# Kernel tuning notes

Hardware: AMD Instinct MI355X
Metric: run time of the kernel (lower is better)

Reference implementation:

```python
import jax, jax.numpy as jnp
import numpy as np

DILS = [2 ** i for i in range(9)] * 7  # 27 residual-only layers + 36 layers with skip
N0 = 27  # first 27 layers (dilations0) do not contribute to skip connections


def _dconv(x, w, b, d):
    # dilated 'same' conv1d: x [B,C,T], w [O,I,3]
    y = jax.lax.conv_general_dilated(x, w, (1,), [(d, d)], rhs_dilation=(d,),
                                     dimension_numbers=('NCH', 'OIH', 'NCH'))
    return y + b[None, :, None]


def _pw(x, w, b):
    # 1x1 conv: w [O,C], x [B,C,T]
    return jnp.einsum('oc,bct->bot', w, x) + b[None, :, None]


def setup_inputs() -> dict:
    key = jax.random.key(0)
    ks = jax.random.split(key, 13)
    B, T, rd, sd, qd, L = 8, 16384, 128, 128, 256, 63
    s = 0.05
    f = lambda k, sh: jax.random.normal(k, sh, jnp.float32) * s
    return {
        'x': jax.random.normal(ks[0], (B, 1, T), jnp.float32),
        'causal_w': f(ks[1], (rd, 1, 25)),
        'causal_b': f(ks[2], (rd,)),
        'dcnn_w': f(ks[3], (L, rd, rd, 3)),
        'dcnn_b': f(ks[4], (L, rd)),
        'dense_w': f(ks[5], (L, rd, rd)),
        'dense_b': f(ks[6], (L, rd)),
        'skip_w': f(ks[7], (L, sd, rd)),
        'skip_b': f(ks[8], (L, sd)),
        'post1_w': f(ks[9], (sd, sd)),
        'post1_b': f(ks[10], (sd,)),
        'post2_w': f(ks[11], (qd, sd)),
        'post2_b': f(ks[12], (qd,)),
    }


def reference(x, causal_w, causal_b, dcnn_w, dcnn_b, dense_w, dense_b,
              skip_w, skip_b, post1_w, post1_b, post2_w, post2_b):
    # causal conv: kernel 25, padding 12 ('same')
    x = jax.lax.conv_general_dilated(x, causal_w, (1,), [(12, 12)],
                                     dimension_numbers=('NCH', 'OIH', 'NCH'))
    x = x + causal_b[None, :, None]
    B, _, T = x.shape
    skip = jnp.zeros((B, skip_w.shape[1], T), x.dtype)
    for cnt, d in enumerate(DILS):
        xin = x
        h = jax.nn.relu(x)
        h = jax.nn.relu(_dconv(h, dcnn_w[cnt], dcnn_b[cnt], d))
        if cnt >= N0:
            skip = skip + _pw(h, skip_w[cnt], skip_b[cnt])
        x = _pw(h, dense_w[cnt], dense_b[cnt]) + xin
    h = jax.nn.relu(_pw(jax.nn.relu(skip), post1_w, post1_b))
    return _pw(h, post2_w, post2_b)
```

## Files before the change

### kernel.cpp

```cpp
#include <hip/hip_runtime.h>

#define RD     128
#define TT     128
#define TLEN   16384
#define NB     8
#define NLAYER 63
#define N0SKIP 27
#define QD     256
#define PADR   136

typedef short bf16x8 __attribute__((ext_vector_type(8)));
typedef float f32x4  __attribute__((ext_vector_type(4)));

__device__ __forceinline__ unsigned short f2bf(float f) {
  unsigned u = __float_as_uint(f);
  u += 0x7fffu + ((u >> 16) & 1u);
  return (unsigned short)(u >> 16);
}
__device__ __forceinline__ short f2bf_relu(float f) {
  f = f > 0.f ? f : 0.f;
  unsigned u = __float_as_uint(f);
  u += 0x7fffu + ((u >> 16) & 1u);
  return (short)(u >> 16);
}

__device__ __forceinline__ void mfma_gemm(const unsigned short* __restrict__ aw,
                                          const short* sx, int rowbase,
                                          int c0w, int t0w, int n, int q,
                                          f32x4 (&acc)[4][4]) {
#pragma unroll
  for (int ks = 0; ks < 4; ++ks) {
    const int i0 = ks * 32 + q * 8;
    bf16x8 a[4], bb[4];
#pragma unroll
    for (int ct = 0; ct < 4; ++ct)
      a[ct] = *(const bf16x8*)&aw[(size_t)(c0w + ct * 16 + n) * RD + i0];
#pragma unroll
    for (int tt = 0; tt < 4; ++tt)
      bb[tt] = *(const bf16x8*)&sx[(rowbase + t0w + tt * 16 + n) * PADR + i0];
#pragma unroll
    for (int ct = 0; ct < 4; ++ct)
#pragma unroll
      for (int tt = 0; tt < 4; ++tt)
        acc[ct][tt] = __builtin_amdgcn_mfma_f32_16x16x32_bf16(a[ct], bb[tt],
                                                              acc[ct][tt], 0, 0, 0);
  }
}

__device__ __forceinline__ void zero_acc(f32x4 (&acc)[4][4]) {
#pragma unroll
  for (int i = 0; i < 4; ++i)
#pragma unroll
    for (int j = 0; j < 4; ++j) acc[i][j] = (f32x4){0.f, 0.f, 0.f, 0.f};
}

__device__ __forceinline__ void stage_rows(short* sx, int rowbase,
                                           const float* __restrict__ xb,
                                           int tstart, int nrows, int tid) {
  for (int idx = tid; idx < nrows * 32; idx += 256) {
    const int r = idx >> 5, c4 = (idx & 31) << 2;
    const int tg = tstart + r;
    float4 v = make_float4(0.f, 0.f, 0.f, 0.f);
    if ((unsigned)tg < (unsigned)TLEN)
      v = *(const float4*)&xb[(size_t)tg * RD + c4];
    short4 o;
    o.x = f2bf_relu(v.x); o.y = f2bf_relu(v.y);
    o.z = f2bf_relu(v.z); o.w = f2bf_relu(v.w);
    *(short4*)&sx[(rowbase + r) * PADR + c4] = o;
  }
}

__device__ __forceinline__ void store_act_bf16(short* dst, const f32x4 (&acc)[4][4],
                                               const float* __restrict__ bias,
                                               int c0w, int t0w, int n, int q) {
#pragma unroll
  for (int ct = 0; ct < 4; ++ct) {
    const int c = c0w + ct * 16 + q * 4;
    const float4 bb = *(const float4*)&bias[c];
#pragma unroll
    for (int tt = 0; tt < 4; ++tt) {
      const int t = t0w + tt * 16 + n;
      const f32x4 A = acc[ct][tt];
      short4 o;
      o.x = f2bf_relu(A[0] + bb.x);
      o.y = f2bf_relu(A[1] + bb.y);
      o.z = f2bf_relu(A[2] + bb.z);
      o.w = f2bf_relu(A[3] + bb.w);
      *(short4*)&dst[t * PADR + c] = o;
    }
  }
}

__device__ __forceinline__ void epi_accum(float* __restrict__ dst,
                                          const float* __restrict__ src,
                                          const float* __restrict__ bias,
                                          const f32x4 (&acc)[4][4],
                                          int c0w, int t0w, int n, int q) {
#pragma unroll
  for (int ct = 0; ct < 4; ++ct) {
    const int c = c0w + ct * 16 + q * 4;
    const float4 bb = *(const float4*)&bias[c];
#pragma unroll
    for (int tt = 0; tt < 4; ++tt) {
      const int t = t0w + tt * 16 + n;
      float4 r = *(const float4*)&src[(size_t)t * RD + c];
      const f32x4 A = acc[ct][tt];
      r.x += A[0] + bb.x; r.y += A[1] + bb.y;
      r.z += A[2] + bb.z; r.w += A[3] + bb.w;
      *(float4*)&dst[(size_t)t * RD + c] = r;
    }
  }
}

__global__ __launch_bounds__(256, 2) void layer_kernel(
    const float* __restrict__ x_in, float* __restrict__ x_out,
    float* __restrict__ skip,
    const unsigned short* __restrict__ wconv,
    const float* __restrict__ bconv,
    const unsigned short* __restrict__ wdense, const float* __restrict__ bdense,
    const unsigned short* __restrict__ wskip,  const float* __restrict__ bskip,
    int dil, int do_skip) {
  __shared__ short sx[256 * PADR];

  const int tid = threadIdx.x;
  const int b   = blockIdx.x >> 7;
  const int t0  = (blockIdx.x & 127) << 7;
  const int lane = tid & 63;
  const int n = lane & 15, q = lane >> 4;
  const int w = tid >> 6;
  const int c0w = (w & 1) * 64, t0w = (w >> 1) * 64;
  const float* xb = x_in + (size_t)b * TLEN * RD;

  f32x4 acc[4][4];
  zero_acc(acc);

  if (dil <= 64) {
    stage_rows(sx, 0, xb, t0 - dil, 128 + 2 * dil, tid);
    __syncthreads();
    for (int k = 0; k < 3; ++k)
      mfma_gemm(wconv + (size_t)k * RD * RD, sx, k * dil, c0w, t0w, n, q, acc);
  } else {
    stage_rows(sx, 0, xb, t0 - dil, 128, tid);
    __syncthreads();
    stage_rows(sx, 128, xb, t0, 128, tid);
    mfma_gemm(wconv, sx, 0, c0w, t0w, n, q, acc);
    __syncthreads();
    stage_rows(sx, 0, xb, t0 + dil, 128, tid);
    mfma_gemm(wconv + (size_t)RD * RD, sx, 128, c0w, t0w, n, q, acc);
    __syncthreads();
    mfma_gemm(wconv + (size_t)2 * RD * RD, sx, 0, c0w, t0w, n, q, acc);
  }
  __syncthreads();

  store_act_bf16(sx, acc, bconv, c0w, t0w, n, q);
  __syncthreads();

  zero_acc(acc);
  mfma_gemm(wdense, sx, 0, c0w, t0w, n, q, acc);
  {
    float* xo = x_out + ((size_t)b * TLEN + t0) * RD;
    const float* xi = x_in + ((size_t)b * TLEN + t0) * RD;
    epi_accum(xo, xi, bdense, acc, c0w, t0w, n, q);
  }

  if (do_skip) {
    zero_acc(acc);
    mfma_gemm(wskip, sx, 0, c0w, t0w, n, q, acc);
    float* sp = skip + ((size_t)b * TLEN + t0) * RD;
    epi_accum(sp, sp, bskip, acc, c0w, t0w, n, q);
  }
}

__global__ __launch_bounds__(256) void causal_kernel(const float* __restrict__ x,
                                                     const float* __restrict__ w,
                                                     const float* __restrict__ bias,
                                                     float* __restrict__ y) {
  __shared__ float xw[152];
  __shared__ float wl[RD * 25];
  __shared__ float bl[RD];
  const int tid = threadIdx.x;
  const int b   = blockIdx.x >> 7;
  const int t0  = (blockIdx.x & 127) << 7;
  for (int i = tid; i < RD * 25; i += 256) wl[i] = w[i];
  if (tid < RD) bl[tid] = bias[tid];
  for (int i = tid; i < 152; i += 256) {
    const int tg = t0 - 12 + i;
    xw[i] = ((unsigned)tg < (unsigned)TLEN) ? x[(size_t)b * TLEN + tg] : 0.f;
  }
  __syncthreads();
  const int c = tid & 127, tp = tid >> 7;
  float* yb = y + ((size_t)b * TLEN + t0) * RD + c;
  const float bc = bl[c];
  for (int i = 0; i < 64; ++i) {
    const int tl = i * 2 + tp;
    float s = bc;
#pragma unroll
    for (int k = 0; k < 25; ++k) s = fmaf(wl[c * 25 + k], xw[tl + k], s);
    yb[(size_t)tl * RD] = s;
  }
}

__global__ __launch_bounds__(256, 1) void post_kernel(
    const float* __restrict__ skip,
    const unsigned short* __restrict__ p1, const float* __restrict__ p1b,
    const unsigned short* __restrict__ p2, const float* __restrict__ p2b,
    float* __restrict__ out) {
  __shared__ short sb[128 * PADR];
  __shared__ short h1[128 * PADR];
  __shared__ float ost[128 * 132];

  const int tid = threadIdx.x;
  const int b   = blockIdx.x >> 7;
  const int t0  = (blockIdx.x & 127) << 7;
  const int lane = tid & 63;
  const int n = lane & 15, q = lane >> 4;
  const int w = tid >> 6;
  const int c0w = (w & 1) * 64, t0w = (w >> 1) * 64;
  const float* skb = skip + ((size_t)b * TLEN + t0) * RD;

  for (int idx = tid; idx < 128 * 32; idx += 256) {
    const int r = idx >> 5, c4 = (idx & 31) << 2;
    float4 v = *(const float4*)&skb[(size_t)r * RD + c4];
    short4 o;
    o.x = f2bf_relu(v.x); o.y = f2bf_relu(v.y);
    o.z = f2bf_relu(v.z); o.w = f2bf_relu(v.w);
    *(short4*)&sb[r * PADR + c4] = o;
  }
  __syncthreads();

  f32x4 acc[4][4];
  zero_acc(acc);
  mfma_gemm(p1, sb, 0, c0w, t0w, n, q, acc);
  store_act_bf16(h1, acc, p1b, c0w, t0w, n, q);
  __syncthreads();

  for (int half = 0; half < 2; ++half) {
    zero_acc(acc);
    mfma_gemm(p2 + (size_t)half * RD * RD, h1, 0, c0w, t0w, n, q, acc);
#pragma unroll
    for (int ct = 0; ct < 4; ++ct) {
      const int c = c0w + ct * 16 + q * 4;
      const float4 bb = *(const float4*)&p2b[half * RD + c];
#pragma unroll
      for (int tt = 0; tt < 4; ++tt) {
        const int t = t0w + tt * 16 + n;
        const f32x4 A = acc[ct][tt];
        ost[(c + 0) * 132 + t] = A[0] + bb.x;
        ost[(c + 1) * 132 + t] = A[1] + bb.y;
        ost[(c + 2) * 132 + t] = A[2] + bb.z;
        ost[(c + 3) * 132 + t] = A[3] + bb.w;
      }
    }
    __syncthreads();
    float* ob = out + ((size_t)b * QD + half * RD) * TLEN + t0;
    for (int idx = tid; idx < 128 * 32; idx += 256) {
      const int r = idx >> 5, t4 = (idx & 31) << 2;
      const float4 v = *(const float4*)&ost[r * 132 + t4];
      *(float4*)&ob[(size_t)r * TLEN + t4] = v;
    }
    __syncthreads();
  }
}

__global__ __launch_bounds__(256) void cvt_kernel(const float* __restrict__ in,
                                                  unsigned short* __restrict__ out,
                                                  int total) {
  const int i = blockIdx.x * 256 + threadIdx.x;
  if (i < total) out[i] = f2bf(in[i]);
}
__global__ __launch_bounds__(256) void cvt_conv_kernel(const float* __restrict__ in,
                                                       unsigned short* __restrict__ out,
                                                       int total) {
  const int idx = blockIdx.x * 256 + threadIdx.x;
  if (idx >= total) return;
  const int ci = idx & 127, co = (idx >> 7) & 127, lk = idx >> 14;
  const int k = lk % 3, l = lk / 3;
  out[idx] = f2bf(in[(((size_t)l * RD + co) * RD + ci) * 3 + k]);
}

extern "C" void kernel_launch(void* const* d_in, const int* in_sizes, int n_in,
                              void* d_out, int out_size, void* d_ws, size_t ws_size,
                              hipStream_t stream) {
  const float* x        = (const float*)d_in[0];
  const float* causal_w = (const float*)d_in[1];
  const float* causal_b = (const float*)d_in[2];
  const float* dcnn_w   = (const float*)d_in[3];
  const float* dcnn_b   = (const float*)d_in[4];
  const float* dense_w  = (const float*)d_in[5];
  const float* dense_b  = (const float*)d_in[6];
  const float* skip_w   = (const float*)d_in[7];
  const float* skip_b   = (const float*)d_in[8];
  const float* post1_w  = (const float*)d_in[9];
  const float* post1_b  = (const float*)d_in[10];
  const float* post2_w  = (const float*)d_in[11];
  const float* post2_b  = (const float*)d_in[12];
  float* out = (float*)d_out;

  const size_t XN = (size_t)NB * TLEN * RD;
  float* ws  = (float*)d_ws;
  float* xA  = ws;
  float* xB  = xA + XN;
  float* skp = xB + XN;
  unsigned short* wc  = (unsigned short*)(skp + XN);
  unsigned short* wd  = wc  + (size_t)NLAYER * 3 * RD * RD;
  unsigned short* wsk = wd  + (size_t)NLAYER * RD * RD;
  unsigned short* p1  = wsk + (size_t)NLAYER * RD * RD;
  unsigned short* p2  = p1  + RD * RD;

  const int tconv = NLAYER * 3 * RD * RD;
  const int t2    = NLAYER * RD * RD;
  cvt_conv_kernel<<<(tconv + 255) / 256, 256, 0, stream>>>(dcnn_w, wc, tconv);
  cvt_kernel<<<(t2 + 255) / 256, 256, 0, stream>>>(dense_w, wd, t2);
  cvt_kernel<<<(t2 + 255) / 256, 256, 0, stream>>>(skip_w, wsk, t2);
  cvt_kernel<<<(RD * RD + 255) / 256, 256, 0, stream>>>(post1_w, p1, RD * RD);
  cvt_kernel<<<(QD * RD + 255) / 256, 256, 0, stream>>>(post2_w, p2, QD * RD);

  causal_kernel<<<NB * (TLEN / TT), 256, 0, stream>>>(x, causal_w, causal_b, xA);
  hipMemsetAsync(skp, 0, XN * sizeof(float), stream);

  const float* src = xA;
  float* dst = xB;
  for (int l = 0; l < NLAYER; ++l) {
    const int dil = 1 << (l % 9);
    layer_kernel<<<NB * (TLEN / TT), 256, 0, stream>>>(
        src, dst, skp,
        wc  + (size_t)l * 3 * RD * RD, dcnn_b  + (size_t)l * RD,
        wd  + (size_t)l * RD * RD,     dense_b + (size_t)l * RD,
        wsk + (size_t)l * RD * RD,     skip_b  + (size_t)l * RD,
        dil, (l >= N0SKIP) ? 1 : 0);
    const float* tmp = src; src = dst; dst = (float*)tmp;
  }

  post_kernel<<<NB * (TLEN / TT), 256, 0, stream>>>(skp, p1, post1_b, p2, post2_b, out);
}
```

Measured before the change: 5.228 ms.

## Shrink LDS staging to raise occupancy, unroll staging loads, swizzle block order

Cuts the shared staging buffer from 256 to 192 rows and raises the launch-bounds occupancy hint from 2 to 3 blocks per CU. To fit, dilation 64 gets its own reuse-based staging path, and larger dilations stage one 128-row tap at a time with extra barriers. The staging loop is unrolled 8 ways so more global loads are in flight, and block IDs are swizzled across batches. The tighter launch bound may force register spills, and the added syncs for large dilations serialize load and compute.

```diff
diff --git a/kernel.cpp b/kernel.cpp
--- a/kernel.cpp
+++ b/kernel.cpp
@@ -8,6 +8,7 @@
 #define N0SKIP 27
 #define QD     256
 #define PADR   136
+#define SROWS  192
 
 typedef short bf16x8 __attribute__((ext_vector_type(8)));
 typedef float f32x4  __attribute__((ext_vector_type(4)));
@@ -54,19 +55,44 @@
     for (int j = 0; j < 4; ++j) acc[i][j] = (f32x4){0.f, 0.f, 0.f, 0.f};
 }
 
+#define SUNROLL 8
 __device__ __forceinline__ void stage_rows(short* sx, int rowbase,
                                            const float* __restrict__ xb,
                                            int tstart, int nrows, int tid) {
-  for (int idx = tid; idx < nrows * 32; idx += 256) {
-    const int r = idx >> 5, c4 = (idx & 31) << 2;
-    const int tg = tstart + r;
+  const int total = nrows * 32;
+  int idx = tid;
+  for (; idx + 256 * (SUNROLL - 1) < total; idx += 256 * SUNROLL) {
+    float4 v[SUNROLL];
+#pragma unroll
+    for (int u = 0; u < SUNROLL; ++u) {
+      const int i2 = idx + u * 256;
+      const int tg = tstart + (i2 >> 5);
+      const int c4 = (i2 & 31) << 2;
+      v[u] = make_float4(0.f, 0.f, 0.f, 0.f);
+      if ((unsigned)tg < (unsigned)TLEN)
+        v[u] = *(const float4*)&xb[(size_t)tg * RD + c4];
+    }
+#pragma unroll
+    for (int u = 0; u < SUNROLL; ++u) {
+      const int i2 = idx + u * 256;
+      const int r = i2 >> 5;
+      const int c4 = (i2 & 31) << 2;
+      short4 o;
+      o.x = f2bf_relu(v[u].x); o.y = f2bf_relu(v[u].y);
+      o.z = f2bf_relu(v[u].z); o.w = f2bf_relu(v[u].w);
+      *(short4*)&sx[(rowbase + r) * PADR + c4] = o;
+    }
+  }
+  for (; idx < total; idx += 256) {
+    const int tg = tstart + (idx >> 5);
+    const int c4 = (idx & 31) << 2;
     float4 v = make_float4(0.f, 0.f, 0.f, 0.f);
     if ((unsigned)tg < (unsigned)TLEN)
       v = *(const float4*)&xb[(size_t)tg * RD + c4];
     short4 o;
     o.x = f2bf_relu(v.x); o.y = f2bf_relu(v.y);
     o.z = f2bf_relu(v.z); o.w = f2bf_relu(v.w);
-    *(short4*)&sx[(rowbase + r) * PADR + c4] = o;
+    *(short4*)&sx[(rowbase + (idx >> 5)) * PADR + c4] = o;
   }
 }
 
@@ -112,7 +138,7 @@
   }
 }
 
-__global__ __launch_bounds__(256, 2) void layer_kernel(
+__global__ __launch_bounds__(256, 3) void layer_kernel(
     const float* __restrict__ x_in, float* __restrict__ x_out,
     float* __restrict__ skip,
     const unsigned short* __restrict__ wconv,
@@ -120,11 +146,13 @@
     const unsigned short* __restrict__ wdense, const float* __restrict__ bdense,
     const unsigned short* __restrict__ wskip,  const float* __restrict__ bskip,
     int dil, int do_skip) {
-  __shared__ short sx[256 * PADR];
+  __shared__ short sx[SROWS * PADR];
 
   const int tid = threadIdx.x;
-  const int b   = blockIdx.x >> 7;
-  const int t0  = (blockIdx.x & 127) << 7;
+  const int bid = blockIdx.x;
+  const int swz = (bid & 7) * 128 + (bid >> 3);
+  const int b   = swz >> 7;
+  const int t0  = (swz & 127) << 7;
   const int lane = tid & 63;
   const int n = lane & 15, q = lane >> 4;
   const int w = tid >> 6;
@@ -134,21 +162,29 @@
   f32x4 acc[4][4];
   zero_acc(acc);
 
-  if (dil <= 64) {
+  if (dil <= 32) {
     stage_rows(sx, 0, xb, t0 - dil, 128 + 2 * dil, tid);
     __syncthreads();
     for (int k = 0; k < 3; ++k)
       mfma_gemm(wconv + (size_t)k * RD * RD, sx, k * dil, c0w, t0w, n, q, acc);
+  } else if (dil == 64) {
+    stage_rows(sx, 0, xb, t0 - 64, 192, tid);
+    __syncthreads();
+    mfma_gemm(wconv, sx, 0, c0w, t0w, n, q, acc);
+    mfma_gemm(wconv + (size_t)RD * RD, sx, 64, c0w, t0w, n, q, acc);
+    __syncthreads();
+    stage_rows(sx, 0, xb, t0 + 128, 64, tid);
+    __syncthreads();
+    mfma_gemm(wconv + (size_t)2 * RD * RD, sx, (t0w == 0) ? 128 : -64,
+              c0w, t0w, n, q, acc);
   } else {
-    stage_rows(sx, 0, xb, t0 - dil, 128, tid);
-    __syncthreads();
-    stage_rows(sx, 128, xb, t0, 128, tid);
-    mfma_gemm(wconv, sx, 0, c0w, t0w, n, q, acc);
-    __syncthreads();
-    stage_rows(sx, 0, xb, t0 + dil, 128, tid);
-    mfma_gemm(wconv + (size_t)RD * RD, sx, 128, c0w, t0w, n, q, acc);
-    __syncthreads();
-    mfma_gemm(wconv + (size_t)2 * RD * RD, sx, 0, c0w, t0w, n, q, acc);
+#pragma unroll
+    for (int k = 0; k < 3; ++k) {
+      stage_rows(sx, 0, xb, t0 + (k - 1) * dil, 128, tid);
+      __syncthreads();
+      mfma_gemm(wconv + (size_t)k * RD * RD, sx, 0, c0w, t0w, n, q, acc);
+      __syncthreads();
+    }
   }
   __syncthreads();
 
```

Result: slower. 8.438 ms (+61.4%).
